# Optimization experiments

Hardware: AMD Instinct MI355X
Metric: run time of the kernel (lower is better)

The kernel has to match this reference:

```python
import jax, jax.numpy as jnp
import numpy as np

B, S, D, H, L, DFF, LAT, V, N = 256, 64, 512, 8, 6, 2048, 256, 16, 64


def _pe(s, d):
    pos = np.arange(s)[:, None].astype(np.float32)
    div = np.exp(np.arange(0, d, 2).astype(np.float32) * (-np.log(10000.0) / d))
    pe = np.zeros((s, d), np.float32)
    pe[:, 0::2] = np.sin(pos * div)
    pe[:, 1::2] = np.cos(pos * div)
    return jnp.asarray(pe)


def setup_inputs() -> dict:
    key = jax.random.key(0)
    ks = iter(jax.random.split(key, 64))
    def nrm(shape, scale):
        return jax.random.normal(next(ks), shape, jnp.float32) * scale
    d = {}
    d['latent'] = nrm((B, LAT), 1.0)
    ct = jax.random.randint(next(ks), (B, S), 0, V).astype(jnp.float32)
    na = jax.random.randint(next(ks), (B, S), 0, N).astype(jnp.float32)
    nb = jax.random.randint(next(ks), (B, S), 0, N).astype(jnp.float32)
    val = jax.random.normal(next(ks), (B, S), jnp.float32)
    d['teacher_seq'] = jnp.stack([ct, na, nb, val], -1)
    for g in ('gumbel_a', 'gumbel_b'):
        u = jax.random.uniform(next(ks), (B, S, N), jnp.float32, 1e-6, 1.0 - 1e-6)
        d[g] = -jnp.log(-jnp.log(u))
    dq = D // 4
    d['type_emb'] = nrm((V, dq), 0.02)
    d['node_a_emb'] = nrm((N, dq), 0.02)
    d['node_b_emb'] = nrm((N, dq), 0.02)
    d['value_w'] = nrm((dq, 1), 1.0); d['value_b'] = jnp.zeros((dq,))
    d['proj_w'] = nrm((D, D), D ** -0.5); d['proj_b'] = jnp.zeros((D,))
    d['latent_w'] = nrm((D, LAT), LAT ** -0.5); d['latent_b'] = jnp.zeros((D,))
    d['sa_in_w'] = nrm((L, 3 * D, D), D ** -0.5); d['sa_in_b'] = jnp.zeros((L, 3 * D))
    d['sa_out_w'] = nrm((L, D, D), D ** -0.5); d['sa_out_b'] = jnp.zeros((L, D))
    d['ca_q_w'] = nrm((L, D, D), D ** -0.5); d['ca_q_b'] = jnp.zeros((L, D))
    d['ca_kv_w'] = nrm((L, 2 * D, D), D ** -0.5); d['ca_kv_b'] = jnp.zeros((L, 2 * D))
    d['ca_out_w'] = nrm((L, D, D), D ** -0.5); d['ca_out_b'] = jnp.zeros((L, D))
    d['ff1_w'] = nrm((L, DFF, D), D ** -0.5); d['ff1_b'] = jnp.zeros((L, DFF))
    d['ff2_w'] = nrm((L, D, DFF), DFF ** -0.5); d['ff2_b'] = jnp.zeros((L, D))
    for nm in ('ln1', 'ln2', 'ln3'):
        d[nm + '_g'] = jnp.ones((L, D)); d[nm + '_b'] = jnp.zeros((L, D))
    d['type_w'] = nrm((V, D), D ** -0.5); d['type_b'] = jnp.zeros((V,))
    d['na_w'] = nrm((N, D), D ** -0.5); d['na_b'] = jnp.zeros((N,))
    d['val_w'] = nrm((1, D), D ** -0.5); d['val_b'] = jnp.zeros((1,))
    d['nb_w'] = nrm((N, D + N), (D + N) ** -0.5); d['nb_b'] = jnp.zeros((N,))
    return d


def _ln(x, g, b, eps=1e-5):
    m = x.mean(-1, keepdims=True)
    v = jnp.mean((x - m) ** 2, -1, keepdims=True)
    return (x - m) / jnp.sqrt(v + eps) * g + b


def _attn(xq, xkv, wq, bq, wk, bk, wv, bv, wo, bo, mask):
    b, sq, dm = xq.shape
    hd = dm // H
    q = (xq @ wq.T + bq).reshape(b, sq, H, hd)
    k = (xkv @ wk.T + bk).reshape(b, -1, H, hd)
    v = (xkv @ wv.T + bv).reshape(b, -1, H, hd)
    s = jnp.einsum('bqhd,bkhd->bhqk', q, k) / np.sqrt(hd).astype(np.float32)
    if mask is not None:
        s = s + mask
    a = jax.nn.softmax(s, -1)
    o = jnp.einsum('bhqk,bkhd->bqhd', a, v).reshape(b, sq, dm)
    return o @ wo.T + bo


def _forward(latent, teacher_seq, gumbel_a, gumbel_b, type_emb, node_a_emb, node_b_emb,
             value_w, value_b, proj_w, proj_b, latent_w, latent_b,
             sa_in_w, sa_in_b, sa_out_w, sa_out_b,
             ca_q_w, ca_q_b, ca_kv_w, ca_kv_b, ca_out_w, ca_out_b,
             ff1_w, ff1_b, ff2_w, ff2_b,
             ln1_g, ln1_b, ln2_g, ln2_b, ln3_g, ln3_b,
             type_w, type_b, na_w, na_b, val_w, val_b, nb_w, nb_b):
    s = teacher_seq.shape[1]
    memory = (latent @ latent_w.T + latent_b)[:, None, :]  # [B,1,D]
    ct = jnp.clip(teacher_seq[..., 0].astype(jnp.int32), 0, V - 1)
    na = jnp.clip(teacher_seq[..., 1].astype(jnp.int32), 0, N - 1)
    nb = jnp.clip(teacher_seq[..., 2].astype(jnp.int32), 0, N - 1)
    emb = jnp.concatenate([type_emb[ct], node_a_emb[na], node_b_emb[nb],
                           teacher_seq[..., 3:4] @ value_w.T + value_b], -1)
    x = emb @ proj_w.T + proj_b + _pe(s, D)
    mask = jnp.where(jnp.triu(jnp.ones((s, s), bool), 1), -jnp.inf, 0.0)
    for l in range(L):
        wq, wk, wv = jnp.split(sa_in_w[l], 3, 0)
        bq, bk, bv = jnp.split(sa_in_b[l], 3, 0)
        x = _ln(x + _attn(x, x, wq, bq, wk, bk, wv, bv, sa_out_w[l], sa_out_b[l], mask), ln1_g[l], ln1_b[l])
        wkc, wvc = jnp.split(ca_kv_w[l], 2, 0)
        bkc, bvc = jnp.split(ca_kv_b[l], 2, 0)
        x = _ln(x + _attn(x, memory, ca_q_w[l], ca_q_b[l], wkc, bkc, wvc, bvc, ca_out_w[l], ca_out_b[l], None), ln2_g[l], ln2_b[l])
        ff = jax.nn.relu(x @ ff1_w[l].T + ff1_b[l]) @ ff2_w[l].T + ff2_b[l]
        x = _ln(x + ff, ln3_g[l], ln3_b[l])
    type_logits = x @ type_w.T + type_b
    node_a_logits = x @ na_w.T + na_b
    values = x @ val_w.T + val_b
    # gumbel_softmax(logits, tau).argmax == argmax(logits + gumbel) (tau > 0)
    node_a_sample = jnp.argmax(node_a_logits + gumbel_a, -1)
    oh = jax.nn.one_hot(node_a_sample, N, dtype=x.dtype)
    node_b_logits = jnp.concatenate([x, oh], -1) @ nb_w.T + nb_b
    masked = jnp.where(oh > 0, -jnp.inf, node_b_logits)  # node_b != node_a constraint
    node_b_sample = jnp.argmax(masked + gumbel_b, -1)
    sequence = jnp.stack([jnp.argmax(type_logits, -1).astype(x.dtype),
                          node_a_sample.astype(x.dtype),
                          node_b_sample.astype(x.dtype),
                          values[..., 0]], -1)
    return type_logits, node_a_logits, node_b_logits, values, sequence


def reference(latent, teacher_seq, gumbel_a, gumbel_b, type_emb, node_a_emb, node_b_emb,
              value_w, value_b, proj_w, proj_b, latent_w, latent_b,
              sa_in_w, sa_in_b, sa_out_w, sa_out_b,
              ca_q_w, ca_q_b, ca_kv_w, ca_kv_b, ca_out_w, ca_out_b,
              ff1_w, ff1_b, ff2_w, ff2_b,
              ln1_g, ln1_b, ln2_g, ln2_b, ln3_g, ln3_b,
              type_w, type_b, na_w, na_b, val_w, val_b, nb_w, nb_b):
    return _forward(latent, teacher_seq, gumbel_a, gumbel_b, type_emb, node_a_emb, node_b_emb,
                    value_w, value_b, proj_w, proj_b, latent_w, latent_b,
                    sa_in_w, sa_in_b, sa_out_w, sa_out_b,
                    ca_q_w, ca_q_b, ca_kv_w, ca_kv_b, ca_out_w, ca_out_b,
                    ff1_w, ff1_b, ff2_w, ff2_b,
                    ln1_g, ln1_b, ln2_g, ln2_b, ln3_g, ln3_b,
                    type_w, type_b, na_w, na_b, val_w, val_b, nb_w, nb_b)
```

## Files before the change

kernel.cpp:

```cpp
#include <hip/hip_runtime.h>
#include <math.h>

#define BB    256
#define SS    64
#define DD    512
#define HH    8
#define LL    6
#define DFFc  2048
#define LATc  256
#define VVc   16
#define NNODE 64
#define TOK   (BB*SS)

typedef __attribute__((ext_vector_type(8))) _Float16 h8v;
typedef __attribute__((ext_vector_type(4))) float f4v;
typedef __attribute__((ext_vector_type(8))) unsigned short u16x8;

__device__ __forceinline__ float pe_val(int s, int c){
  const float kc = -9.2103403719761836f / 512.0f;
  float div = expf((float)(c & ~1) * kc);
  float arg = (float)s * div;
  return (c & 1) ? cosf(arg) : sinf(arg);
}

__device__ __forceinline__ unsigned short hbits(_Float16 h){
  union { _Float16 h; unsigned short u; } x; x.h = h; return x.u;
}
__device__ __forceinline__ void split4h(float4 v, ushort4& h0, ushort4& h1){
  _Float16 a0 = (_Float16)v.x; float r0 = v.x - (float)a0; h0.x = hbits(a0); h1.x = hbits((_Float16)r0);
  _Float16 a1 = (_Float16)v.y; float r1 = v.y - (float)a1; h0.y = hbits(a1); h1.y = hbits((_Float16)r1);
  _Float16 a2 = (_Float16)v.z; float r2 = v.z - (float)a2; h0.z = hbits(a2); h1.z = hbits((_Float16)r2);
  _Float16 a3 = (_Float16)v.w; float r3 = v.w - (float)a3; h0.w = hbits(a3); h1.w = hbits((_Float16)r3);
}
__device__ __forceinline__ u16x8 pack8(ushort4 a, ushort4 b){
  u16x8 r;
  r[0]=a.x; r[1]=a.y; r[2]=a.z; r[3]=a.w;
  r[4]=b.x; r[5]=b.y; r[6]=b.z; r[7]=b.w;
  return r;
}

__global__ __launch_bounds__(128) void emb_kernel(
    const float* __restrict__ ts, const float* __restrict__ te,
    const float* __restrict__ nae, const float* __restrict__ nbe,
    const float* __restrict__ vw, const float* __restrict__ vb,
    float* __restrict__ emb)
{
  const int tok = blockIdx.x;
  const int d   = threadIdx.x;
  float c0  = ts[(size_t)tok*4 + 0];
  float c1  = ts[(size_t)tok*4 + 1];
  float c2  = ts[(size_t)tok*4 + 2];
  float val = ts[(size_t)tok*4 + 3];
  int ct = min(max((int)c0, 0), VVc - 1);
  int na = min(max((int)c1, 0), NNODE - 1);
  int nb = min(max((int)c2, 0), NNODE - 1);
  float* er = emb + (size_t)tok * DD;
  er[d]       = te [ct*128 + d];
  er[128 + d] = nae[na*128 + d];
  er[256 + d] = nbe[nb*128 + d];
  er[384 + d] = val * vw[d] + vb[d];
}

template<int RELU, int ADDPE>
__global__ __launch_bounds__(256) void gemm_mfma(
    const float* __restrict__ A, const float* __restrict__ W,
    const float* __restrict__ bias, float* __restrict__ Cc,
    int M, int N, int K)
{
  __shared__ __attribute__((aligned(16))) unsigned short Ab[2][128][32];
  __shared__ __attribute__((aligned(16))) unsigned short Bb[2][128][32];
  const int n0 = blockIdx.x * 128;
  const int m0 = blockIdx.y * 128;
  const int t  = threadIdx.x;
  const int lane = t & 63;
  const int wave = t >> 6;
  const int wr = (wave >> 1) * 64;
  const int wc = (wave & 1) * 64;
  const int quad = lane >> 4;
  const int lc   = lane & 15;

  const int srow = t >> 1;
  const int skh  = (t & 1) * 16;

  const int ssw = ((srow ^ (srow >> 2)) & 3);
  const int p0  = (((t & 1) * 2) ^ ssw) * 8;
  const int p1  = ((((t & 1) * 2) ^ ssw) ^ 1) * 8;
  const int fo  = ((quad ^ ((lc ^ (lc >> 2)) & 3))) * 8;

  const float* ap = A + (size_t)(m0 + srow) * K + skh;
  const float* wp = W + (size_t)(n0 + srow) * K + skh;

  f4v acc[4][4];
  #pragma unroll
  for (int i = 0; i < 4; ++i)
    #pragma unroll
    for (int j = 0; j < 4; ++j) acc[i][j] = (f4v){0.f, 0.f, 0.f, 0.f};

  float4 va[4], vb[4];
  #pragma unroll
  for (int q = 0; q < 4; ++q) {
    va[q] = *(const float4*)(ap + q*4);
    vb[q] = *(const float4*)(wp + q*4);
  }

  for (int k0 = 0; k0 < K; k0 += 32) {
    __syncthreads();
    {
      ushort4 h0[4], h1[4];
      #pragma unroll
      for (int q = 0; q < 4; ++q) split4h(va[q], h0[q], h1[q]);
      *(u16x8*)&Ab[0][srow][p0] = pack8(h0[0], h0[1]);
      *(u16x8*)&Ab[0][srow][p1] = pack8(h0[2], h0[3]);
      *(u16x8*)&Ab[1][srow][p0] = pack8(h1[0], h1[1]);
      *(u16x8*)&Ab[1][srow][p1] = pack8(h1[2], h1[3]);
      #pragma unroll
      for (int q = 0; q < 4; ++q) split4h(vb[q], h0[q], h1[q]);
      *(u16x8*)&Bb[0][srow][p0] = pack8(h0[0], h0[1]);
      *(u16x8*)&Bb[0][srow][p1] = pack8(h0[2], h0[3]);
      *(u16x8*)&Bb[1][srow][p0] = pack8(h1[0], h1[1]);
      *(u16x8*)&Bb[1][srow][p1] = pack8(h1[2], h1[3]);
    }
    __syncthreads();
    if (k0 + 32 < K) {
      #pragma unroll
      for (int q = 0; q < 4; ++q) {
        va[q] = *(const float4*)(ap + k0 + 32 + q*4);
        vb[q] = *(const float4*)(wp + k0 + 32 + q*4);
      }
    }
    h8v af[2][4];
    #pragma unroll
    for (int mt = 0; mt < 4; ++mt)
      #pragma unroll
      for (int s = 0; s < 2; ++s)
        af[s][mt] = *(const h8v*)&Ab[s][wr + mt*16 + lc][fo];
    #pragma unroll
    for (int nt = 0; nt < 4; ++nt) {
      h8v b0 = *(const h8v*)&Bb[0][wc + nt*16 + lc][fo];
      h8v b1 = *(const h8v*)&Bb[1][wc + nt*16 + lc][fo];
      #pragma unroll
      for (int mt = 0; mt < 4; ++mt) {
        f4v c = acc[mt][nt];
        c = __builtin_amdgcn_mfma_f32_16x16x32_f16(af[1][mt], b0, c, 0, 0, 0);
        c = __builtin_amdgcn_mfma_f32_16x16x32_f16(af[0][mt], b1, c, 0, 0, 0);
        c = __builtin_amdgcn_mfma_f32_16x16x32_f16(af[0][mt], b0, c, 0, 0, 0);
        acc[mt][nt] = c;
      }
    }
  }
  #pragma unroll
  for (int mt = 0; mt < 4; ++mt)
    #pragma unroll
    for (int nt = 0; nt < 4; ++nt) {
      int col = n0 + wc + nt*16 + lc;
      float bvv = bias ? bias[col] : 0.f;
      #pragma unroll
      for (int r = 0; r < 4; ++r) {
        int row = m0 + wr + mt*16 + quad*4 + r;
        float v = acc[mt][nt][r] + bvv;
        if (RELU)  v = fmaxf(v, 0.f);
        if (ADDPE) v += pe_val(row & (SS - 1), col);
        Cc[(size_t)row * N + col] = v;
      }
    }
}

template<int RELU, int ADDPE>
__global__ __launch_bounds__(256) void gemm_mfma64(
    const float* __restrict__ A, const float* __restrict__ W,
    const float* __restrict__ bias, float* __restrict__ Cc,
    int M, int N, int K)
{
  __shared__ __attribute__((aligned(16))) unsigned short Ab[2][64][32];
  __shared__ __attribute__((aligned(16))) unsigned short Bb[2][128][32];
  const int n0 = blockIdx.x * 128;
  const int m0 = blockIdx.y * 64;
  const int t  = threadIdx.x;
  const int lane = t & 63;
  const int wave = t >> 6;
  const int wr = (wave >> 1) * 32;
  const int wc = (wave & 1) * 64;
  const int quad = lane >> 4;
  const int lc   = lane & 15;

  const int srow = t >> 1;
  const int skh  = (t & 1) * 16;
  const int ssw  = ((srow ^ (srow >> 2)) & 3);
  const int p0   = (((t & 1) * 2) ^ ssw) * 8;
  const int p1   = ((((t & 1) * 2) ^ ssw) ^ 1) * 8;
  const int arow = t >> 2;
  const int aq   = t & 3;
  const int pA   = (aq ^ ((arow ^ (arow >> 2)) & 3)) * 8;
  const int fo   = ((quad ^ ((lc ^ (lc >> 2)) & 3))) * 8;

  const float* ap = A + (size_t)(m0 + arow) * K + aq*8;
  const float* wp = W + (size_t)(n0 + srow) * K + skh;

  f4v acc[2][4];
  #pragma unroll
  for (int i = 0; i < 2; ++i)
    #pragma unroll
    for (int j = 0; j < 4; ++j) acc[i][j] = (f4v){0.f, 0.f, 0.f, 0.f};

  float4 va[2], vb[4];
  va[0] = *(const float4*)(ap);
  va[1] = *(const float4*)(ap + 4);
  #pragma unroll
  for (int q = 0; q < 4; ++q) vb[q] = *(const float4*)(wp + q*4);

  for (int k0 = 0; k0 < K; k0 += 32) {
    __syncthreads();
    {
      ushort4 h0[4], h1[4];
      split4h(va[0], h0[0], h1[0]);
      split4h(va[1], h0[1], h1[1]);
      *(u16x8*)&Ab[0][arow][pA] = pack8(h0[0], h0[1]);
      *(u16x8*)&Ab[1][arow][pA] = pack8(h1[0], h1[1]);
      #pragma unroll
      for (int q = 0; q < 4; ++q) split4h(vb[q], h0[q], h1[q]);
      *(u16x8*)&Bb[0][srow][p0] = pack8(h0[0], h0[1]);
      *(u16x8*)&Bb[0][srow][p1] = pack8(h0[2], h0[3]);
      *(u16x8*)&Bb[1][srow][p0] = pack8(h1[0], h1[1]);
      *(u16x8*)&Bb[1][srow][p1] = pack8(h1[2], h1[3]);
    }
    __syncthreads();
    if (k0 + 32 < K) {
      va[0] = *(const float4*)(ap + k0 + 32);
      va[1] = *(const float4*)(ap + k0 + 36);
      #pragma unroll
      for (int q = 0; q < 4; ++q) vb[q] = *(const float4*)(wp + k0 + 32 + q*4);
    }
    h8v af[2][2];
    #pragma unroll
    for (int mt = 0; mt < 2; ++mt)
      #pragma unroll
      for (int s = 0; s < 2; ++s)
        af[s][mt] = *(const h8v*)&Ab[s][wr + mt*16 + lc][fo];
    #pragma unroll
    for (int nt = 0; nt < 4; ++nt) {
      h8v b0 = *(const h8v*)&Bb[0][wc + nt*16 + lc][fo];
      h8v b1 = *(const h8v*)&Bb[1][wc + nt*16 + lc][fo];
      #pragma unroll
      for (int mt = 0; mt < 2; ++mt) {
        f4v c = acc[mt][nt];
        c = __builtin_amdgcn_mfma_f32_16x16x32_f16(af[1][mt], b0, c, 0, 0, 0);
        c = __builtin_amdgcn_mfma_f32_16x16x32_f16(af[0][mt], b1, c, 0, 0, 0);
        c = __builtin_amdgcn_mfma_f32_16x16x32_f16(af[0][mt], b0, c, 0, 0, 0);
        acc[mt][nt] = c;
      }
    }
  }
  #pragma unroll
  for (int mt = 0; mt < 2; ++mt)
    #pragma unroll
    for (int nt = 0; nt < 4; ++nt) {
      int col = n0 + wc + nt*16 + lc;
      float bvv = bias ? bias[col] : 0.f;
      #pragma unroll
      for (int r = 0; r < 4; ++r) {
        int row = m0 + wr + mt*16 + quad*4 + r;
        float v = acc[mt][nt][r] + bvv;
        if (RELU)  v = fmaxf(v, 0.f);
        if (ADDPE) v += pe_val(row & (SS - 1), col);
        Cc[(size_t)row * N + col] = v;
      }
    }
}

__global__ __launch_bounds__(256) void gemm64(
    const float* __restrict__ A, const float* __restrict__ W,
    const float* __restrict__ bias, float* __restrict__ Cc,
    int M, int N, int K)
{
  __shared__ float As[16][64];
  __shared__ float Bs[16][64];
  const int n0 = blockIdx.x * 64;
  const int m0 = blockIdx.y * 64;
  const int t  = threadIdx.x;
  const int tx = t & 15;
  const int ty = t >> 4;
  const int sr = t >> 2;
  const int sk = (t & 3) * 4;

  const float* ap = A + (size_t)(m0 + sr) * K + sk;
  const float* wp = W + (size_t)(n0 + sr) * K + sk;

  float acc[4][4];
  #pragma unroll
  for (int i = 0; i < 4; ++i)
    #pragma unroll
    for (int j = 0; j < 4; ++j) acc[i][j] = 0.f;

  float4 a = *(const float4*)ap;
  float4 b = *(const float4*)wp;
  for (int k0 = 0; k0 < K; k0 += 16) {
    __syncthreads();
    As[sk+0][sr]=a.x; As[sk+1][sr]=a.y; As[sk+2][sr]=a.z; As[sk+3][sr]=a.w;
    Bs[sk+0][sr]=b.x; Bs[sk+1][sr]=b.y; Bs[sk+2][sr]=b.z; Bs[sk+3][sr]=b.w;
    __syncthreads();
    if (k0 + 16 < K) {
      a = *(const float4*)(ap + k0 + 16);
      b = *(const float4*)(wp + k0 + 16);
    }
    #pragma unroll
    for (int kk = 0; kk < 16; ++kk) {
      float4 x = *(const float4*)&As[kk][ty*4];
      float4 y = *(const float4*)&Bs[kk][tx*4];
      float xv[4] = {x.x,x.y,x.z,x.w};
      float yv[4] = {y.x,y.y,y.z,y.w};
      #pragma unroll
      for (int i = 0; i < 4; ++i)
        #pragma unroll
        for (int j = 0; j < 4; ++j)
          acc[i][j] += xv[i] * yv[j];
    }
  }
  #pragma unroll
  for (int i = 0; i < 4; ++i) {
    int r = m0 + ty*4 + i;
    float* cp = Cc + (size_t)r * N + n0 + tx*4;
    float4 o;
    o.x = acc[i][0] + (bias ? bias[n0+tx*4+0] : 0.f);
    o.y = acc[i][1] + (bias ? bias[n0+tx*4+1] : 0.f);
    o.z = acc[i][2] + (bias ? bias[n0+tx*4+2] : 0.f);
    o.w = acc[i][3] + (bias ? bias[n0+tx*4+3] : 0.f);
    *(float4*)cp = o;
  }
}

__global__ __launch_bounds__(64) void attn_kernel(
    const float* __restrict__ qkv, float* __restrict__ out)
{
  const int b = blockIdx.x >> 3;
  const int h = blockIdx.x & 7;
  const int lane = threadIdx.x;
  __shared__ float4 ks[64][16];
  __shared__ float4 vs[64][16];
  const float* base = qkv + (size_t)(b*SS + lane) * (3*DD);
  #pragma unroll
  for (int dd = 0; dd < 16; ++dd) {
    ks[lane][dd] = *(const float4*)(base + DD     + h*64 + dd*4);
    vs[lane][dd] = *(const float4*)(base + 2*DD   + h*64 + dd*4);
  }
  float4 q4[16];
  #pragma unroll
  for (int dd = 0; dd < 16; ++dd) q4[dd] = *(const float4*)(base + h*64 + dd*4);
  __syncthreads();

  float s[64];
  float m = -1e30f;
  #pragma unroll
  for (int tk = 0; tk < 64; ++tk) {
    float acc = 0.f;
    #pragma unroll
    for (int dd = 0; dd < 16; ++dd) {
      float4 kv = ks[tk][dd];
      acc += q4[dd].x*kv.x + q4[dd].y*kv.y + q4[dd].z*kv.z + q4[dd].w*kv.w;
    }
    acc *= 0.125f;
    s[tk] = acc;
    if (tk <= lane && acc > m) m = acc;
  }
  float4 o4[16];
  #pragma unroll
  for (int dd = 0; dd < 16; ++dd) { o4[dd].x = 0.f; o4[dd].y = 0.f; o4[dd].z = 0.f; o4[dd].w = 0.f; }
  float l = 0.f;
  #pragma unroll
  for (int tk = 0; tk < 64; ++tk) {
    float w = (tk <= lane) ? expf(s[tk] - m) : 0.f;
    l += w;
    #pragma unroll
    for (int dd = 0; dd < 16; ++dd) {
      float4 vv = vs[tk][dd];
      o4[dd].x += w*vv.x; o4[dd].y += w*vv.y; o4[dd].z += w*vv.z; o4[dd].w += w*vv.w;
    }
  }
  float inv = 1.f / l;
  float* op = out + (size_t)(b*SS + lane) * DD + h*64;
  #pragma unroll
  for (int dd = 0; dd < 16; ++dd) {
    float4 vv; vv.x = o4[dd].x*inv; vv.y = o4[dd].y*inv; vv.z = o4[dd].z*inv; vv.w = o4[dd].w*inv;
    *(float4*)(op + dd*4) = vv;
  }
}

__global__ __launch_bounds__(256) void ln_kernel(
    float* __restrict__ x, const float* __restrict__ y,
    const float* __restrict__ g, const float* __restrict__ b, int ybcast)
{
  const int tok  = blockIdx.x * 4 + (threadIdx.x >> 6);
  const int lane = threadIdx.x & 63;
  float* xr = x + (size_t)tok * DD;
  const float* yr = y + (size_t)(ybcast ? (tok >> 6) : tok) * DD;
  const int c0 = lane * 8;
  float4 v0 = *(const float4*)(xr + c0);
  float4 v1 = *(const float4*)(xr + c0 + 4);
  float4 y0 = *(const float4*)(yr + c0);
  float4 y1 = *(const float4*)(yr + c0 + 4);
  float v[8] = {v0.x+y0.x, v0.y+y0.y, v0.z+y0.z, v0.w+y0.w,
                v1.x+y1.x, v1.y+y1.y, v1.z+y1.z, v1.w+y1.w};
  float sum = 0.f;
  #pragma unroll
  for (int i = 0; i < 8; ++i) sum += v[i];
  #pragma unroll
  for (int off = 32; off; off >>= 1) sum += __shfl_xor(sum, off);
  float mean = sum * (1.f / 512.f);
  float ss = 0.f;
  #pragma unroll
  for (int i = 0; i < 8; ++i) { float d = v[i] - mean; ss += d*d; }
  #pragma unroll
  for (int off = 32; off; off >>= 1) ss += __shfl_xor(ss, off);
  float rinv = 1.f / sqrtf(ss * (1.f / 512.f) + 1e-5f);
  float4 g0 = *(const float4*)(g + c0);
  float4 g1 = *(const float4*)(g + c0 + 4);
  float4 b0 = *(const float4*)(b + c0);
  float4 b1 = *(const float4*)(b + c0 + 4);
  float4 o0, o1;
  o0.x = (v[0]-mean)*rinv*g0.x + b0.x;
  o0.y = (v[1]-mean)*rinv*g0.y + b0.y;
  o0.z = (v[2]-mean)*rinv*g0.z + b0.z;
  o0.w = (v[3]-mean)*rinv*g0.w + b0.w;
  o1.x = (v[4]-mean)*rinv*g1.x + b1.x;
  o1.y = (v[5]-mean)*rinv*g1.y + b1.y;
  o1.z = (v[6]-mean)*rinv*g1.z + b1.z;
  o1.w = (v[7]-mean)*rinv*g1.w + b1.w;
  *(float4*)(xr + c0)     = o0;
  *(float4*)(xr + c0 + 4) = o1;
}

__global__ __launch_bounds__(128) void build_whead(
    const float* __restrict__ tw, const float* __restrict__ tb,
    const float* __restrict__ nw, const float* __restrict__ nab,
    const float* __restrict__ bw, const float* __restrict__ bbb,
    const float* __restrict__ vw, const float* __restrict__ vb,
    float* __restrict__ Wh, float* __restrict__ Bh)
{
  const int row = blockIdx.x;
  const int t   = threadIdx.x;
  const float* src = nullptr; float bias = 0.f;
  if      (row < 16)  { src = tw + (size_t)row*512;        bias = tb[row]; }
  else if (row < 80)  { src = nw + (size_t)(row-16)*512;   bias = nab[row-16]; }
  else if (row < 144) { src = bw + (size_t)(row-80)*576;   bias = bbb[row-80]; }
  else if (row == 144){ src = vw;                          bias = vb[0]; }
  float* dst = Wh + (size_t)row*512;
  const int c = t * 4;
  float4 v;
  if (src) v = *(const float4*)(src + c);
  else { v.x = 0.f; v.y = 0.f; v.z = 0.f; v.w = 0.f; }
  *(float4*)(dst + c) = v;
  if (t == 0) Bh[row] = bias;
}

__device__ __forceinline__ void argmax64(float& v, int& idx){
  #pragma unroll
  for (int off = 1; off < 64; off <<= 1) {
    float ov = __shfl_xor(v, off);
    int   oi = __shfl_xor(idx, off);
    if (ov > v || (ov == v && oi < idx)) { v = ov; idx = oi; }
  }
}

__global__ __launch_bounds__(64) void head_finalize(
    const float* __restrict__ LG, const float* __restrict__ nb_w,
    const float* __restrict__ gum_a, const float* __restrict__ gum_b,
    float* __restrict__ out)
{
  const int O_NA  = TOK*VVc;
  const int O_NB  = O_NA + TOK*NNODE;
  const int O_VAL = O_NB + TOK*NNODE;
  const int O_SEQ = O_VAL + TOK;
  const int tok  = blockIdx.x;
  const int lane = threadIdx.x;
  const float* lg = LG + (size_t)tok * 256;

  float tl = (lane < VVc) ? lg[lane] : -INFINITY;
  if (lane < VVc) out[(size_t)tok*VVc + lane] = tl;
  float tv = tl; int ti = lane;
  argmax64(tv, ti);

  float nl = lg[16 + lane];
  out[O_NA + (size_t)tok*NNODE + lane] = nl;
  float av = nl + gum_a[(size_t)tok*NNODE + lane];
  int ai = lane;
  argmax64(av, ai);

  float bl = lg[80 + lane] + nb_w[(size_t)lane*576 + 512 + ai];
  out[O_NB + (size_t)tok*NNODE + lane] = bl;
  float mb = (lane == ai) ? -INFINITY : bl;
  mb += gum_b[(size_t)tok*NNODE + lane];
  int bi = lane;
  argmax64(mb, bi);

  if (lane == 0) {
    float value = lg[144];
    out[O_VAL + tok]               = value;
    out[O_SEQ + (size_t)tok*4 + 0] = (float)ti;
    out[O_SEQ + (size_t)tok*4 + 1] = (float)ai;
    out[O_SEQ + (size_t)tok*4 + 2] = (float)bi;
    out[O_SEQ + (size_t)tok*4 + 3] = value;
  }
}

__device__ __forceinline__ float dot512(const float* __restrict__ xs, const float* __restrict__ w){
  float s = 0.f;
  #pragma unroll 8
  for (int k = 0; k < 512; k += 4) {
    float4 u = *(const float4*)(w + k);
    s += xs[k]*u.x + xs[k+1]*u.y + xs[k+2]*u.z + xs[k+3]*u.w;
  }
  return s;
}

__global__ __launch_bounds__(64) void head_kernel(
    const float* __restrict__ x,
    const float* __restrict__ type_w, const float* __restrict__ type_b,
    const float* __restrict__ na_w,  const float* __restrict__ na_b,
    const float* __restrict__ vw,    const float* __restrict__ vb,
    const float* __restrict__ nb_w,  const float* __restrict__ nb_b,
    const float* __restrict__ gum_a, const float* __restrict__ gum_b,
    float* __restrict__ out)
{
  const int O_NA  = TOK*VVc;
  const int O_NB  = O_NA + TOK*NNODE;
  const int O_VAL = O_NB + TOK*NNODE;
  const int O_SEQ = O_VAL + TOK;
  const int tok  = blockIdx.x;
  const int lane = threadIdx.x;
  __shared__ float xs[512];
  const float* xr = x + (size_t)tok * DD;
  *(float4*)&xs[lane*8]     = *(const float4*)(xr + lane*8);
  *(float4*)&xs[lane*8 + 4] = *(const float4*)(xr + lane*8 + 4);
  __syncthreads();

  float pv = 0.f;
  #pragma unroll
  for (int i = 0; i < 8; ++i) pv += xs[lane*8 + i] * vw[lane*8 + i];
  #pragma unroll
  for (int off = 32; off; off >>= 1) pv += __shfl_xor(pv, off);
  float value = pv + vb[0];

  float tl = -INFINITY;
  if (lane < VVc) {
    tl = type_b[lane] + dot512(xs, type_w + (size_t)lane*512);
    out[(size_t)tok*VVc + lane] = tl;
  }
  float tv = tl; int ti = lane;
  argmax64(tv, ti);

  float nl = na_b[lane] + dot512(xs, na_w + (size_t)lane*512);
  out[O_NA + (size_t)tok*NNODE + lane] = nl;
  float av = nl + gum_a[(size_t)tok*NNODE + lane];
  int ai = lane;
  argmax64(av, ai);

  const float* wr = nb_w + (size_t)lane * 576;
  float bl = nb_b[lane] + dot512(xs, wr) + wr[512 + ai];
  out[O_NB + (size_t)tok*NNODE + lane] = bl;
  float mb = (lane == ai) ? -INFINITY : bl;
  mb += gum_b[(size_t)tok*NNODE + lane];
  int bi = lane;
  argmax64(mb, bi);

  if (lane == 0) {
    out[O_VAL + tok]               = value;
    out[O_SEQ + (size_t)tok*4 + 0] = (float)ti;
    out[O_SEQ + (size_t)tok*4 + 1] = (float)ai;
    out[O_SEQ + (size_t)tok*4 + 2] = (float)bi;
    out[O_SEQ + (size_t)tok*4 + 3] = value;
  }
}

extern "C" void kernel_launch(void* const* d_in, const int* in_sizes, int n_in,
                              void* d_out, int out_size, void* d_ws, size_t ws_size,
                              hipStream_t stream)
{
  (void)in_sizes; (void)n_in; (void)out_size;
  const float* latent   = (const float*)d_in[0];
  const float* teacher  = (const float*)d_in[1];
  const float* gum_a    = (const float*)d_in[2];
  const float* gum_b    = (const float*)d_in[3];
  const float* type_emb = (const float*)d_in[4];
  const float* nae      = (const float*)d_in[5];
  const float* nbe      = (const float*)d_in[6];
  const float* value_w  = (const float*)d_in[7];
  const float* value_b  = (const float*)d_in[8];
  const float* proj_w   = (const float*)d_in[9];
  const float* proj_b   = (const float*)d_in[10];
  const float* latent_w = (const float*)d_in[11];
  const float* latent_b = (const float*)d_in[12];
  const float* sa_in_w  = (const float*)d_in[13];
  const float* sa_in_b  = (const float*)d_in[14];
  const float* sa_out_w = (const float*)d_in[15];
  const float* sa_out_b = (const float*)d_in[16];
  const float* ca_kv_w  = (const float*)d_in[19];
  const float* ca_kv_b  = (const float*)d_in[20];
  const float* ca_out_w = (const float*)d_in[21];
  const float* ca_out_b = (const float*)d_in[22];
  const float* ff1_w    = (const float*)d_in[23];
  const float* ff1_b    = (const float*)d_in[24];
  const float* ff2_w    = (const float*)d_in[25];
  const float* ff2_b    = (const float*)d_in[26];
  const float* ln1_g    = (const float*)d_in[27];
  const float* ln1_b    = (const float*)d_in[28];
  const float* ln2_g    = (const float*)d_in[29];
  const float* ln2_b    = (const float*)d_in[30];
  const float* ln3_g    = (const float*)d_in[31];
  const float* ln3_b    = (const float*)d_in[32];
  const float* type_w   = (const float*)d_in[33];
  const float* type_b   = (const float*)d_in[34];
  const float* na_w     = (const float*)d_in[35];
  const float* na_b     = (const float*)d_in[36];
  const float* val_w    = (const float*)d_in[37];
  const float* val_b    = (const float*)d_in[38];
  const float* nb_w     = (const float*)d_in[39];
  const float* nb_b     = (const float*)d_in[40];

  int C = 128;
  for (int c = 16384; c >= 128; c >>= 1) {
    size_t need = ((size_t)8781824 + (size_t)3072 * c) * 4;
    if (need <= ws_size) { C = c; break; }
  }
  const int NCH = TOK / C;

  float* ws   = (float*)d_ws;
  float* X    = ws;
  float* U    = X    + (size_t)TOK*DD;
  float* P1   = U    + (size_t)2048*C;
  float* P2   = P1   + (size_t)C*DD;
  float* MEM  = P2   + (size_t)C*DD;
  float* CAV  = MEM  + (size_t)BB*DD;
  float* CAO  = CAV  + (size_t)BB*DD;
  float* out = (float*)d_out;

  for (int c = 0; c < NCH; ++c) {
    emb_kernel<<<C, 128, 0, stream>>>(teacher + (size_t)c*C*4, type_emb, nae, nbe, value_w, value_b, U);
    gemm_mfma64<0,1><<<dim3(DD/128, C/64), 256, 0, stream>>>(U, proj_w, proj_b, X + (size_t)c*C*DD, C, DD, DD);
  }
  gemm64<<<dim3(DD/64, BB/64), 256, 0, stream>>>(latent, latent_w, latent_b, MEM, BB, DD, LATc);

  for (int l = 0; l < LL; ++l) {
    const float* w_qkv = sa_in_w  + (size_t)l*3*DD*DD;
    const float* b_qkv = sa_in_b  + (size_t)l*3*DD;
    const float* w_so  = sa_out_w + (size_t)l*DD*DD;
    const float* b_so  = sa_out_b + (size_t)l*DD;
    const float* w_cv  = ca_kv_w  + (size_t)l*2*DD*DD + (size_t)DD*DD;
    const float* b_cv  = ca_kv_b  + (size_t)l*2*DD + DD;
    const float* w_co  = ca_out_w + (size_t)l*DD*DD;
    const float* b_co  = ca_out_b + (size_t)l*DD;
    const float* w_f1  = ff1_w    + (size_t)l*DFFc*DD;
    const float* b_f1  = ff1_b    + (size_t)l*DFFc;
    const float* w_f2  = ff2_w    + (size_t)l*DD*DFFc;
    const float* b_f2  = ff2_b    + (size_t)l*DD;

    for (int c = 0; c < NCH; ++c) {
      float* Xc = X + (size_t)c*C*DD;
      gemm_mfma<0,0><<<dim3(3*DD/128, C/128), 256, 0, stream>>>(Xc, w_qkv, b_qkv, U, C, 3*DD, DD);
      attn_kernel<<<(C/SS)*HH, 64, 0, stream>>>(U, P1);
      gemm_mfma64<0,0><<<dim3(DD/128, C/64), 256, 0, stream>>>(P1, w_so, b_so, P2, C, DD, DD);
      ln_kernel<<<C/4, 256, 0, stream>>>(Xc, P2, ln1_g + (size_t)l*DD, ln1_b + (size_t)l*DD, 0);
    }
    gemm64<<<dim3(DD/64, BB/64), 256, 0, stream>>>(MEM, w_cv, b_cv, CAV, BB, DD, DD);
    gemm64<<<dim3(DD/64, BB/64), 256, 0, stream>>>(CAV, w_co, b_co, CAO, BB, DD, DD);
    ln_kernel<<<TOK/4, 256, 0, stream>>>(X, CAO, ln2_g + (size_t)l*DD, ln2_b + (size_t)l*DD, 1);
    for (int c = 0; c < NCH; ++c) {
      float* Xc = X + (size_t)c*C*DD;
      gemm_mfma<1,0><<<dim3(DFFc/128, C/128), 256, 0, stream>>>(Xc, w_f1, b_f1, U, C, DFFc, DD);
      gemm_mfma64<0,0><<<dim3(DD/128, C/64), 256, 0, stream>>>(U, w_f2, b_f2, P1, C, DD, DFFc);
      ln_kernel<<<C/4, 256, 0, stream>>>(Xc, P1, ln3_g + (size_t)l*DD, ln3_b + (size_t)l*DD, 0);
    }
  }

  if (C >= 2048) {
    float* Wh = CAV;
    float* Bh = CAO;
    float* LG = U;
    build_whead<<<256, 128, 0, stream>>>(type_w, type_b, na_w, na_b, nb_w, nb_b, val_w, val_b, Wh, Bh);
    gemm_mfma64<0,0><<<dim3(256/128, TOK/64), 256, 0, stream>>>(X, Wh, Bh, LG, TOK, 256, 512);
    head_finalize<<<TOK, 64, 0, stream>>>(LG, nb_w, gum_a, gum_b, out);
  } else {
    head_kernel<<<TOK, 64, 0, stream>>>(X, type_w, type_b, na_w, na_b, val_w, val_b,
                                        nb_w, nb_b, gum_a, gum_b, out);
  }
}
```

Baseline: 4.000 ms.

## Presplit weights to fp16 pairs, load via global_load_lds, batch cross-attention GEMMs

Adds a presplit kernel that converts fp32 weights into hi/lo fp16 planes once per layer. gemm_mfma64 then streams B tiles straight into LDS with global_load_lds instead of splitting them per tile in registers. The per-layer cross-attention memory GEMMs are hoisted out of the layer loop into batched z-dimension launches. This trades extra presplit launches and a larger workspace for less per-tile conversion work and fewer small launches. The B tile loses its XOR swizzle, so LDS bank conflicts may rise.

Result: slower. 4.618 ms (+15.4%).

```diff
diff --git a/kernel.cpp b/kernel.cpp
--- a/kernel.cpp
+++ b/kernel.cpp
@@ -37,6 +37,25 @@
   r[0]=a.x; r[1]=a.y; r[2]=a.z; r[3]=a.w;
   r[4]=b.x; r[5]=b.y; r[6]=b.z; r[7]=b.w;
   return r;
+}
+
+__device__ __forceinline__ void gload_lds16(const unsigned short* g, unsigned short* l){
+  __builtin_amdgcn_global_load_lds(
+      (const __attribute__((address_space(1))) unsigned int*)g,
+      (__attribute__((address_space(3))) unsigned int*)l,
+      16, 0, 0);
+}
+
+__global__ __launch_bounds__(256) void presplit_w(
+    const float* __restrict__ W, unsigned short* __restrict__ Wp, int nk)
+{
+  const size_t NK = (size_t)nk;
+  const size_t i  = ((size_t)blockIdx.x * 256 + threadIdx.x) * 4;
+  float4 v = *(const float4*)(W + i);
+  ushort4 h0, h1;
+  split4h(v, h0, h1);
+  *(ushort4*)&Wp[i]      = h0;
+  *(ushort4*)&Wp[NK + i] = h1;
 }
 
 __global__ __launch_bounds__(128) void emb_kernel(
@@ -167,7 +186,7 @@
 
 template<int RELU, int ADDPE>
 __global__ __launch_bounds__(256) void gemm_mfma64(
-    const float* __restrict__ A, const float* __restrict__ W,
+    const float* __restrict__ A, const unsigned short* __restrict__ Wp,
     const float* __restrict__ bias, float* __restrict__ Cc,
     int M, int N, int K)
 {
@@ -183,18 +202,31 @@
   const int quad = lane >> 4;
   const int lc   = lane & 15;
 
-  const int srow = t >> 1;
-  const int skh  = (t & 1) * 16;
-  const int ssw  = ((srow ^ (srow >> 2)) & 3);
-  const int p0   = (((t & 1) * 2) ^ ssw) * 8;
-  const int p1   = ((((t & 1) * 2) ^ ssw) ^ 1) * 8;
   const int arow = t >> 2;
   const int aq   = t & 3;
   const int pA   = (aq ^ ((arow ^ (arow >> 2)) & 3)) * 8;
   const int fo   = ((quad ^ ((lc ^ (lc >> 2)) & 3))) * 8;
 
+  const size_t NK = (size_t)N * K;
+  const unsigned short* srcB0; const unsigned short* srcB1;
+  const unsigned short* srcB2; const unsigned short* srcB3;
+  {
+    int g0 = wave*256 + 0*64 + lane;
+    int g1 = wave*256 + 1*64 + lane;
+    int g2 = wave*256 + 2*64 + lane;
+    int g3 = wave*256 + 3*64 + lane;
+    srcB0 = Wp + (size_t)(g0>>9)*NK + (size_t)(n0 + ((g0&511)>>2))*K + (g0&3)*8;
+    srcB1 = Wp + (size_t)(g1>>9)*NK + (size_t)(n0 + ((g1&511)>>2))*K + (g1&3)*8;
+    srcB2 = Wp + (size_t)(g2>>9)*NK + (size_t)(n0 + ((g2&511)>>2))*K + (g2&3)*8;
+    srcB3 = Wp + (size_t)(g3>>9)*NK + (size_t)(n0 + ((g3&511)>>2))*K + (g3&3)*8;
+  }
+  unsigned short* const bbase = &Bb[0][0][0];
+  unsigned short* const dst0 = bbase + (size_t)(wave*256 + 0*64)*8;
+  unsigned short* const dst1 = bbase + (size_t)(wave*256 + 1*64)*8;
+  unsigned short* const dst2 = bbase + (size_t)(wave*256 + 2*64)*8;
+  unsigned short* const dst3 = bbase + (size_t)(wave*256 + 3*64)*8;
+
   const float* ap = A + (size_t)(m0 + arow) * K + aq*8;
-  const float* wp = W + (size_t)(n0 + srow) * K + skh;
 
   f4v acc[2][4];
   #pragma unroll
@@ -202,33 +234,27 @@
     #pragma unroll
     for (int j = 0; j < 4; ++j) acc[i][j] = (f4v){0.f, 0.f, 0.f, 0.f};
 
-  float4 va[2], vb[4];
+  float4 va[2];
   va[0] = *(const float4*)(ap);
   va[1] = *(const float4*)(ap + 4);
-  #pragma unroll
-  for (int q = 0; q < 4; ++q) vb[q] = *(const float4*)(wp + q*4);
 
   for (int k0 = 0; k0 < K; k0 += 32) {
     __syncthreads();
+    gload_lds16(srcB0 + k0, dst0);
+    gload_lds16(srcB1 + k0, dst1);
+    gload_lds16(srcB2 + k0, dst2);
+    gload_lds16(srcB3 + k0, dst3);
     {
-      ushort4 h0[4], h1[4];
-      split4h(va[0], h0[0], h1[0]);
-      split4h(va[1], h0[1], h1[1]);
-      *(u16x8*)&Ab[0][arow][pA] = pack8(h0[0], h0[1]);
-      *(u16x8*)&Ab[1][arow][pA] = pack8(h1[0], h1[1]);
-      #pragma unroll
-      for (int q = 0; q < 4; ++q) split4h(vb[q], h0[q], h1[q]);
-      *(u16x8*)&Bb[0][srow][p0] = pack8(h0[0], h0[1]);
-      *(u16x8*)&Bb[0][srow][p1] = pack8(h0[2], h0[3]);
-      *(u16x8*)&Bb[1][srow][p0] = pack8(h1[0], h1[1]);
-      *(u16x8*)&Bb[1][srow][p1] = pack8(h1[2], h1[3]);
+      ushort4 h0a, h1a, h0b, h1b;
+      split4h(va[0], h0a, h1a);
+      split4h(va[1], h0b, h1b);
+      *(u16x8*)&Ab[0][arow][pA] = pack8(h0a, h0b);
+      *(u16x8*)&Ab[1][arow][pA] = pack8(h1a, h1b);
     }
     __syncthreads();
     if (k0 + 32 < K) {
       va[0] = *(const float4*)(ap + k0 + 32);
       va[1] = *(const float4*)(ap + k0 + 36);
-      #pragma unroll
-      for (int q = 0; q < 4; ++q) vb[q] = *(const float4*)(wp + k0 + 32 + q*4);
     }
     h8v af[2][2];
     #pragma unroll
@@ -238,8 +264,8 @@
         af[s][mt] = *(const h8v*)&Ab[s][wr + mt*16 + lc][fo];
     #pragma unroll
     for (int nt = 0; nt < 4; ++nt) {
-      h8v b0 = *(const h8v*)&Bb[0][wc + nt*16 + lc][fo];
-      h8v b1 = *(const h8v*)&Bb[1][wc + nt*16 + lc][fo];
+      h8v b0 = *(const h8v*)&Bb[0][wc + nt*16 + lc][quad*8];
+      h8v b1 = *(const h8v*)&Bb[1][wc + nt*16 + lc][quad*8];
       #pragma unroll
       for (int mt = 0; mt < 2; ++mt) {
         f4v c = acc[mt][nt];
@@ -267,11 +293,19 @@
     }
 }
 
-__global__ __launch_bounds__(256) void gemm64(
-    const float* __restrict__ A, const float* __restrict__ W,
-    const float* __restrict__ bias, float* __restrict__ Cc,
+__global__ __launch_bounds__(256) void gemm64b(
+    const float* __restrict__ A, long aStr,
+    const float* __restrict__ W, long wStr,
+    const float* __restrict__ bias, long bStr,
+    float* __restrict__ Cc, long cStr,
     int M, int N, int K)
 {
+  const int z = blockIdx.z;
+  A    += (size_t)z * aStr;
+  W    += (size_t)z * wStr;
+  bias += (size_t)z * bStr;
+  Cc   += (size_t)z * cStr;
+
   __shared__ float As[16][64];
   __shared__ float Bs[16][64];
   const int n0 = blockIdx.x * 64;
@@ -433,7 +467,7 @@
     const float* __restrict__ nw, const float* __restrict__ nab,
     const float* __restrict__ bw, const float* __restrict__ bbb,
     const float* __restrict__ vw, const float* __restrict__ vb,
-    float* __restrict__ Wh, float* __restrict__ Bh)
+    unsigned short* __restrict__ Whp, float* __restrict__ Bh)
 {
   const int row = blockIdx.x;
   const int t   = threadIdx.x;
@@ -442,12 +476,15 @@
   else if (row < 80)  { src = nw + (size_t)(row-16)*512;   bias = nab[row-16]; }
   else if (row < 144) { src = bw + (size_t)(row-80)*576;   bias = bbb[row-80]; }
   else if (row == 144){ src = vw;                          bias = vb[0]; }
-  float* dst = Wh + (size_t)row*512;
   const int c = t * 4;
   float4 v;
   if (src) v = *(const float4*)(src + c);
   else { v.x = 0.f; v.y = 0.f; v.z = 0.f; v.w = 0.f; }
-  *(float4*)(dst + c) = v;
+  ushort4 h0, h1;
+  split4h(v, h0, h1);
+  const size_t P = (size_t)256 * 512;
+  *(ushort4*)&Whp[(size_t)row*512 + c]     = h0;
+  *(ushort4*)&Whp[P + (size_t)row*512 + c] = h1;
   if (t == 0) Bh[row] = bias;
 }
 
@@ -617,65 +654,68 @@
 
   int C = 128;
   for (int c = 16384; c >= 128; c >>= 1) {
-    size_t need = ((size_t)8781824 + (size_t)3072 * c) * 4;
+    size_t need = ((size_t)11141120 + (size_t)3072 * c) * 4;
     if (need <= ws_size) { C = c; break; }
   }
   const int NCH = TOK / C;
 
-  float* ws   = (float*)d_ws;
-  float* X    = ws;
-  float* U    = X    + (size_t)TOK*DD;
-  float* P1   = U    + (size_t)2048*C;
-  float* P2   = P1   + (size_t)C*DD;
-  float* MEM  = P2   + (size_t)C*DD;
-  float* CAV  = MEM  + (size_t)BB*DD;
-  float* CAO  = CAV  + (size_t)BB*DD;
+  float* ws     = (float*)d_ws;
+  float* X      = ws;
+  float* U      = X      + (size_t)TOK*DD;
+  float* P1     = U      + (size_t)2048*C;
+  float* P2     = P1     + (size_t)C*DD;
+  float* MEM    = P2     + (size_t)C*DD;
+  float* CAVall = MEM    + (size_t)BB*DD;
+  float* CAOall = CAVall + (size_t)LL*BB*DD;
+  unsigned short* WSP = (unsigned short*)(CAOall + (size_t)LL*BB*DD);
   float* out = (float*)d_out;
 
+  presplit_w<<<512*512/1024, 256, 0, stream>>>(proj_w, WSP, 512*512);
   for (int c = 0; c < NCH; ++c) {
     emb_kernel<<<C, 128, 0, stream>>>(teacher + (size_t)c*C*4, type_emb, nae, nbe, value_w, value_b, U);
-    gemm_mfma64<0,1><<<dim3(DD/128, C/64), 256, 0, stream>>>(U, proj_w, proj_b, X + (size_t)c*C*DD, C, DD, DD);
-  }
-  gemm64<<<dim3(DD/64, BB/64), 256, 0, stream>>>(latent, latent_w, latent_b, MEM, BB, DD, LATc);
+    gemm_mfma64<0,1><<<dim3(DD/128, C/64), 256, 0, stream>>>(U, WSP, proj_b, X + (size_t)c*C*DD, C, DD, DD);
+  }
+  gemm64b<<<dim3(DD/64, BB/64, 1), 256, 0, stream>>>(latent, 0, latent_w, 0, latent_b, 0, MEM, 0, BB, DD, LATc);
+  gemm64b<<<dim3(DD/64, BB/64, LL), 256, 0, stream>>>(
+      MEM, 0, ca_kv_w + (size_t)DD*DD, (long)2*DD*DD, ca_kv_b + DD, (long)2*DD,
+      CAVall, (long)BB*DD, BB, DD, DD);
+  gemm64b<<<dim3(DD/64, BB/64, LL), 256, 0, stream>>>(
+      CAVall, (long)BB*DD, ca_out_w, (long)DD*DD, ca_out_b, (long)DD,
+      CAOall, (long)BB*DD, BB, DD, DD);
 
   for (int l = 0; l < LL; ++l) {
     const float* w_qkv = sa_in_w  + (size_t)l*3*DD*DD;
     const float* b_qkv = sa_in_b  + (size_t)l*3*DD;
     const float* w_so  = sa_out_w + (size_t)l*DD*DD;
     const float* b_so  = sa_out_b + (size_t)l*DD;
-    const float* w_cv  = ca_kv_w  + (size_t)l*2*DD*DD + (size_t)DD*DD;
-    const float* b_cv  = ca_kv_b  + (size_t)l*2*DD + DD;
-    const float* w_co  = ca_out_w + (size_t)l*DD*DD;
-    const float* b_co  = ca_out_b + (size_t)l*DD;
     const float* w_f1  = ff1_w    + (size_t)l*DFFc*DD;
     const float* b_f1  = ff1_b    + (size_t)l*DFFc;
     const float* w_f2  = ff2_w    + (size_t)l*DD*DFFc;
     const float* b_f2  = ff2_b    + (size_t)l*DD;
 
+    presplit_w<<<512*512/1024, 256, 0, stream>>>(w_so, WSP, 512*512);
     for (int c = 0; c < NCH; ++c) {
       float* Xc = X + (size_t)c*C*DD;
       gemm_mfma<0,0><<<dim3(3*DD/128, C/128), 256, 0, stream>>>(Xc, w_qkv, b_qkv, U, C, 3*DD, DD);
       attn_kernel<<<(C/SS)*HH, 64, 0, stream>>>(U, P1);
-      gemm_mfma64<0,0><<<dim3(DD/128, C/64), 256, 0, stream>>>(P1, w_so, b_so, P2, C, DD, DD);
+      gemm_mfma64<0,0><<<dim3(DD/128, C/64), 256, 0, stream>>>(P1, WSP, b_so, P2, C, DD, DD);
       ln_kernel<<<C/4, 256, 0, stream>>>(Xc, P2, ln1_g + (size_t)l*DD, ln1_b + (size_t)l*DD, 0);
     }
-    gemm64<<<dim3(DD/64, BB/64), 256, 0, stream>>>(MEM, w_cv, b_cv, CAV, BB, DD, DD);
-    gemm64<<<dim3(DD/64, BB/64), 256, 0, stream>>>(CAV, w_co, b_co, CAO, BB, DD, DD);
-    ln_kernel<<<TOK/4, 256, 0, stream>>>(X, CAO, ln2_g + (size_t)l*DD, ln2_b + (size_t)l*DD, 1);
+    ln_kernel<<<TOK/4, 256, 0, stream>>>(X, CAOall + (size_t)l*BB*DD, ln2_g + (size_t)l*DD, ln2_b + (size_t)l*DD, 1);
+    presplit_w<<<512*2048/1024, 256, 0, stream>>>(w_f2, WSP, 512*2048);
     for (int c = 0; c < NCH; ++c) {
       float* Xc = X + (size_t)c*C*DD;
       gemm_mfma<1,0><<<dim3(DFFc/128, C/128), 256, 0, stream>>>(Xc, w_f1, b_f1, U, C, DFFc, DD);
-      gemm_mfma64<0,0><<<dim3(DD/128, C/64), 256, 0, stream>>>(U, w_f2, b_f2, P1, C, DD, DFFc);
+      gemm_mfma64<0,0><<<dim3(DD/128, C/64), 256, 0, stream>>>(U, WSP, b_f2, P1, C, DD, DFFc);
       ln_kernel<<<C/4, 256, 0, stream>>>(Xc, P1, ln3_g + (size_t)l*DD, ln3_b + (size_t)l*DD, 0);
     }
   }
 
   if (C >= 2048) {
-    float* Wh = CAV;
-    float* Bh = CAO;
+    float* Bh = CAVall;
     float* LG = U;
-    build_whead<<<256, 128, 0, stream>>>(type_w, type_b, na_w, na_b, nb_w, nb_b, val_w, val_b, Wh, Bh);
-    gemm_mfma64<0,0><<<dim3(256/128, TOK/64), 256, 0, stream>>>(X, Wh, Bh, LG, TOK, 256, 512);
+    build_whead<<<256, 128, 0, stream>>>(type_w, type_b, na_w, na_b, nb_w, nb_b, val_w, val_b, WSP, Bh);
+    gemm_mfma64<0,0><<<dim3(256/128, TOK/64), 256, 0, stream>>>(X, WSP, Bh, LG, TOK, 256, 512);
     head_finalize<<<TOK, 64, 0, stream>>>(LG, nb_w, gum_a, gum_b, out);
   } else {
     head_kernel<<<TOK, 64, 0, stream>>>(X, type_w, type_b, na_w, na_b, val_w, val_b,
```
